# Kernel tuning notes

Hardware: AMD Instinct MI355X
Metric: run time of the kernel (lower is better)

The kernel has to match this reference:

```python
import jax, jax.numpy as jnp
import numpy as np

KS = {0: (6, 18), 1: (4, 12)}


def _build_modal_edges(feat, k_set):
    # feat: [N, C] -> H_modal [N, len(k_set)*N]
    N = feat.shape[0]
    f = feat / jnp.linalg.norm(feat, axis=1, keepdims=True).clip(1e-12)
    sim = f @ f.T  # [N, N] cosine similarity
    H_list = []
    cols_base = jnp.arange(N)
    for k in k_set:
        _, knn = jax.lax.top_k(sim, k + 1)  # [N, k+1]
        rows = knn.reshape(-1)
        cols = jnp.repeat(cols_base, k + 1)
        H = jnp.zeros((N, N), dtype=feat.dtype).at[rows, cols].set(1.0)
        H_list.append(H)
    return jnp.concatenate(H_list, axis=1)


def _build_incidence(feat1, feat2):
    # feat1/feat2: [N, C] (batch-mean features) -> H [2N, 5N]
    N = feat1.shape[0]
    H1 = _build_modal_edges(feat1, KS[0])  # [N, 2N]
    H2 = _build_modal_edges(feat2, KS[1])  # [N, 2N]
    E1, E2 = H1.shape[1], H2.shape[1]
    blk = jnp.concatenate([
        jnp.concatenate([H1, jnp.zeros((N, E2), H1.dtype)], axis=1),
        jnp.concatenate([jnp.zeros((N, E1), H2.dtype), H2], axis=1),
    ], axis=0)  # block_diag -> [2N, 4N]
    eye = jnp.eye(N, dtype=H1.dtype)
    H_inter = jnp.concatenate([eye, eye], axis=0)  # [2N, N]
    return jnp.concatenate([blk, H_inter], axis=1)  # [2N, 5N]


def _hgconv(x, H, W):
    # x: [B, 2N, Fin], H: [2N, E], W: [Fout, Fin] (torch Linear, no bias)
    x = jnp.einsum('bnf,of->bno', x, W)
    DV = H.sum(axis=1).clip(1.0)  # [2N]
    DE = H.sum(axis=0).clip(1.0)  # [E]
    H_norm = H / jnp.sqrt(DV)[:, None] / DE[None, :]
    A = H_norm @ H_norm.T  # [2N, 2N]
    x = jnp.einsum('nm,bmo->bno', A, x)
    return jax.nn.relu(x)


def setup_inputs() -> dict:
    key = jax.random.key(0)
    k1, k2, k3, k4 = jax.random.split(key, 4)
    B, N, C, Hd = 4, 2048, 64, 128
    feat_mod1 = jax.random.normal(k1, (B, N, C), dtype=jnp.float32)
    feat_mod2 = jax.random.normal(k2, (B, N, C), dtype=jnp.float32)
    # xavier_uniform bounds for [out, in]
    b1 = float(np.sqrt(6.0 / (Hd + C)))
    b2 = float(np.sqrt(6.0 / (Hd + Hd)))
    W1 = jax.random.uniform(k3, (Hd, C), minval=-b1, maxval=b1, dtype=jnp.float32)
    W2 = jax.random.uniform(k4, (Hd, Hd), minval=-b2, maxval=b2, dtype=jnp.float32)
    return {"feat_mod1": feat_mod1, "feat_mod2": feat_mod2, "W1": W1, "W2": W2}


def reference(feat_mod1, feat_mod2, W1, W2):
    B, N, _ = feat_mod1.shape
    H = jax.lax.stop_gradient(
        _build_incidence(feat_mod1.mean(axis=0), feat_mod2.mean(axis=0)))
    x = jnp.concatenate([feat_mod1, feat_mod2], axis=1)  # [B, 2N, C]
    x = _hgconv(x, H, W1)
    x = _hgconv(x, H, W2)
    return x[:, :N, :], x[:, N:, :]
```

## Files before the change

kernel.cpp:

```cpp
#include <hip/hip_runtime.h>
#include <math.h>

#define NN 2048
#define TWO_N 4096
#define BB 4
#define CC 64
#define HD 128
#define CANDCAP 32

typedef unsigned short u16;
typedef _Float16 h16;
union H4 { ushort4 u; h16 h[4]; };

__device__ __forceinline__ u16 f2bf(float x) {
    unsigned u = __float_as_uint(x);
    u += 0x7FFFu + ((u >> 16) & 1u);
    return (u16)(u >> 16);
}

__global__ void k_mean_norm(const float* __restrict__ f1, const float* __restrict__ f2,
                            const float* __restrict__ W1, const float* __restrict__ W2,
                            float* __restrict__ g32T, double* __restrict__ gR64,
                            u16* __restrict__ xh,
                            float* __restrict__ W1T, float* __restrict__ W2T,
                            int* __restrict__ DV) {
    int n = blockIdx.x;
    int m = blockIdx.y;
    int c = threadIdx.x;
    if (m == 0 && n < 64) DV[n * 64 + c] = 0;
    if (m == 1) {
        if (n < 128) {
            int idx = n * 64 + c;
            W1T[(size_t)(idx & 63) * HD + (idx >> 6)] = W1[idx];
        } else if (n < 384) {
            int idx = (n - 128) * 64 + c;
            W2T[(size_t)(idx & 127) * HD + (idx >> 7)] = W2[idx];
        }
    }
    const float* f = m ? f2 : f1;
    float xv[BB];
    double s = 0.0;
    for (int b = 0; b < BB; ++b) {
        float v = f[((size_t)(b * NN) + n) * CC + c];
        xv[b] = v; s += (double)v;
    }
    h16* xrow = (h16*)(xh + ((size_t)(m * NN + n)) * (BB * CC));
    for (int b = 0; b < BB; ++b) xrow[b * CC + c] = (h16)xv[b];
    double mean = s * 0.25;
    double sq = mean * mean;
    for (int d = 32; d >= 1; d >>= 1) sq += __shfl_xor(sq, d);
    double norm = sqrt(sq);
    if (norm < 1e-12) norm = 1e-12;
    double g = mean / norm;
    g32T[((size_t)m * CC + c) * NN + n] = (float)g;
    gR64[((size_t)m * NN + n) * CC + c] = g;
}

__global__ void __launch_bounds__(256)
k_sims(const float* __restrict__ g32T, u16* __restrict__ simsbf) {
    __shared__ float As[64 * 64];
    __shared__ float Bs[64 * 64];
    int m  = blockIdx.y;
    int bi = blockIdx.x >> 5, bj = blockIdx.x & 31;
    if (bi > bj) return;
    int i0 = bi * 64, j0 = bj * 64;
    const float* g = g32T + (size_t)m * CC * NN;
    int tid = threadIdx.x;
    #pragma unroll
    for (int q = 0; q < 16; ++q) {
        int idx = q * 256 + tid;
        int k = idx >> 6, r = idx & 63;
        As[k * 64 + r] = g[(size_t)k * NN + i0 + r];
        Bs[k * 64 + r] = g[(size_t)k * NN + j0 + r];
    }
    __syncthreads();
    int tr = tid >> 4, tc = tid & 15;
    float acc[4][4] = {{0.f}};
    #pragma unroll
    for (int k = 0; k < CC; ++k) {
        float4 a = *((const float4*)&As[k * 64 + (tr << 2)]);
        float4 b = *((const float4*)&Bs[k * 64 + (tc << 2)]);
        acc[0][0] += a.x * b.x; acc[0][1] += a.x * b.y; acc[0][2] += a.x * b.z; acc[0][3] += a.x * b.w;
        acc[1][0] += a.y * b.x; acc[1][1] += a.y * b.y; acc[1][2] += a.y * b.z; acc[1][3] += a.y * b.w;
        acc[2][0] += a.z * b.x; acc[2][1] += a.z * b.y; acc[2][2] += a.z * b.z; acc[2][3] += a.z * b.w;
        acc[3][0] += a.w * b.x; acc[3][1] += a.w * b.y; acc[3][2] += a.w * b.z; acc[3][3] += a.w * b.w;
    }
    __syncthreads();
    u16* Cs = (u16*)As;
    u16* srow = simsbf + (size_t)m * NN * NN;
    #pragma unroll
    for (int x = 0; x < 4; ++x) {
        ushort4 vd;
        vd.x = f2bf(acc[x][0]); vd.y = f2bf(acc[x][1]);
        vd.z = f2bf(acc[x][2]); vd.w = f2bf(acc[x][3]);
        *((ushort4*)&srow[(size_t)(i0 + (tr << 2) + x) * NN + j0 + (tc << 2)]) = vd;
        int cr = ((tr << 2) + x) * 66 + (tc << 2);
        Cs[cr + 0] = vd.x; Cs[cr + 1] = vd.y; Cs[cr + 2] = vd.z; Cs[cr + 3] = vd.w;
    }
    __syncthreads();
    #pragma unroll
    for (int q = 0; q < 4; ++q) {
        int idx = q * 256 + tid;
        int cc = idx >> 4, rr4 = (idx & 15) << 2;
        ushort4 vd;
        vd.x = Cs[(rr4 + 0) * 66 + cc];
        vd.y = Cs[(rr4 + 1) * 66 + cc];
        vd.z = Cs[(rr4 + 2) * 66 + cc];
        vd.w = Cs[(rr4 + 3) * 66 + cc];
        *((ushort4*)&srow[(size_t)(j0 + cc) * NN + i0 + rr4]) = vd;
    }
}

__global__ void __launch_bounds__(512)
k_selref(const u16* __restrict__ simsbf, const double* __restrict__ gR64,
         int* __restrict__ knn1, int* __restrict__ knn2, int* __restrict__ DV) {
    __shared__ int    candL[8][CANDCAP];
    __shared__ double dotsL[8][CANDCAP];
    int wave = threadIdx.x >> 6, lane = threadIdx.x & 63;
    int row = blockIdx.x * 8 + wave;
    int m = row >> 11, i = row & 2047;
    int K = m ? 13 : 19;
    const u16* s = simsbf + (size_t)m * NN * NN + (size_t)i * NN;
    float sv[32];
    #pragma unroll
    for (int q = 0; q < 4; ++q) {
        uint4 w = *((const uint4*)(s + q * 512 + (lane << 3)));
        sv[q*8+0] = __uint_as_float(w.x << 16);
        sv[q*8+1] = __uint_as_float(w.x & 0xFFFF0000u);
        sv[q*8+2] = __uint_as_float(w.y << 16);
        sv[q*8+3] = __uint_as_float(w.y & 0xFFFF0000u);
        sv[q*8+4] = __uint_as_float(w.z << 16);
        sv[q*8+5] = __uint_as_float(w.z & 0xFFFF0000u);
        sv[q*8+6] = __uint_as_float(w.w << 16);
        sv[q*8+7] = __uint_as_float(w.w & 0xFFFF0000u);
    }
    float lo = -1.01f, hi = 1.01f;
    for (int it = 0; it < 12; ++it) {
        float t = 0.5f * (lo + hi);
        int c = 0;
        #pragma unroll
        for (int r = 0; r < 32; ++r)
            c += __popcll(__ballot(sv[r] >= t));
        if (c >= K) lo = t; else hi = t;
    }
    float thr = lo - 6e-3f;
    unsigned long long ltmask = (lane == 0) ? 0ull : ((~0ull) >> (64 - lane));
    int base = 0;
    #pragma unroll
    for (int r = 0; r < 32; ++r) {
        int j = ((r >> 3) << 9) + (lane << 3) + (r & 7);
        bool p = sv[r] >= thr;
        unsigned long long mk = __ballot(p);
        int ofs = base + __popcll(mk & ltmask);
        if (p && ofs < CANDCAP) candL[wave][ofs] = j;
        base += __popcll(mk);
    }
    int cnt = (base < CANDCAP) ? base : CANDCAP;
    __syncthreads();
    const double* gm = gR64 + (size_t)m * NN * CC;
    double qc = gm[(size_t)i * CC + lane];
    int t4 = 0;
    for (; t4 + 3 < cnt; t4 += 4) {
        int j0c = candL[wave][t4 + 0], j1c = candL[wave][t4 + 1];
        int j2c = candL[wave][t4 + 2], j3c = candL[wave][t4 + 3];
        double p0 = qc * gm[(size_t)j0c * CC + lane];
        double p1 = qc * gm[(size_t)j1c * CC + lane];
        double p2 = qc * gm[(size_t)j2c * CC + lane];
        double p3 = qc * gm[(size_t)j3c * CC + lane];
        #pragma unroll
        for (int d = 32; d >= 1; d >>= 1) {
            p0 += __shfl_xor(p0, d); p1 += __shfl_xor(p1, d);
            p2 += __shfl_xor(p2, d); p3 += __shfl_xor(p3, d);
        }
        if (lane == 0) {
            dotsL[wave][t4 + 0] = p0; dotsL[wave][t4 + 1] = p1;
            dotsL[wave][t4 + 2] = p2; dotsL[wave][t4 + 3] = p3;
        }
    }
    for (; t4 < cnt; ++t4) {
        int j = candL[wave][t4];
        double p = qc * gm[(size_t)j * CC + lane];
        #pragma unroll
        for (int d = 32; d >= 1; d >>= 1) p += __shfl_xor(p, d);
        if (lane == 0) dotsL[wave][t4] = p;
    }
    __syncthreads();
    int* knn = m ? knn2 : knn1;
    if (lane < cnt) {
        double vt = dotsL[wave][lane]; int jt = candL[wave][lane];
        int rank = 0;
        for (int s2 = 0; s2 < cnt; ++s2) {
            double vs = dotsL[wave][s2]; int js = candL[wave][s2];
            if (vs > vt || (vs == vt && js < jt)) ++rank;
        }
        if (rank < K) {
            knn[(size_t)i * K + rank] = jt;
            int w = (rank < (m ? 5 : 7)) ? 2 : 1;
            atomicAdd(&DV[m ? NN + jt : jt], w);
        }
    }
}

__global__ void k_scan(const int* __restrict__ DV, int* __restrict__ offs,
                       int* __restrict__ cursor, float* __restrict__ dvisf) {
    int lane = threadIdx.x;
    int base = lane * 64;
    int s = 0;
    for (int q = 0; q < 64; ++q) s += DV[base + q];
    int x = s;
    for (int d = 1; d < 64; d <<= 1) {
        int y = __shfl_up(x, d);
        if (lane >= d) x += y;
    }
    int run = x - s;
    for (int q = 0; q < 64; ++q) {
        int v = base + q;
        offs[v] = run; cursor[v] = run;
        dvisf[v] = (float)(1.0 / sqrt((double)(DV[v] + 1)));
        run += DV[v];
    }
    if (lane == 63) offs[TWO_N] = run;
}

__global__ void k_fill(const int* __restrict__ knn1, const int* __restrict__ knn2,
                       int* __restrict__ cursor, int* __restrict__ entries) {
    int id = blockIdx.x * blockDim.x + threadIdx.x;
    const int M1 = NN * 19, M2 = NN * 13;
    if (id < M1) {
        int i = id / 19, t = id % 19;
        int v = knn1[id];
        int p = atomicAdd(&cursor[v], 1); entries[p] = NN + i;
        if (t < 7) { int p2 = atomicAdd(&cursor[v], 1); entries[p2] = i; }
    } else if (id < M1 + M2) {
        int id2 = id - M1;
        int i = id2 / 13, t = id2 % 13;
        int v = NN + knn2[id2];
        int p = atomicAdd(&cursor[v], 1); entries[p] = 3 * NN + i;
        if (t < 5) { int p2 = atomicAdd(&cursor[v], 1); entries[p2] = 2 * NN + i; }
    }
}

__global__ void k_edgeX(const u16* __restrict__ xh, const float* __restrict__ dvisf,
                        const int* __restrict__ knn1, const int* __restrict__ knn2,
                        u16* __restrict__ uh1) {
    int blk = blockIdx.x;
    int t = threadIdx.x;
    int off = t * 4;
    if (blk < NN) {
        int mv = 0; float wv = 0.f;
        if (t < 19) { mv = knn1[(size_t)blk * 19 + t]; wv = dvisf[mv]; }
        float a0=0,a1=0,a2=0,a3=0;
        #pragma unroll
        for (int q = 0; q < 7; ++q) {
            int mq = __shfl(mv, q); float wq = __shfl(wv, q);
            H4 hv; hv.u = *((const ushort4*)(xh + (size_t)mq * 256 + off));
            a0 += (float)hv.h[0]*wq; a1 += (float)hv.h[1]*wq;
            a2 += (float)hv.h[2]*wq; a3 += (float)hv.h[3]*wq;
        }
        { H4 ho; ho.h[0]=(h16)(a0*(1.f/49.f)); ho.h[1]=(h16)(a1*(1.f/49.f));
          ho.h[2]=(h16)(a2*(1.f/49.f)); ho.h[3]=(h16)(a3*(1.f/49.f));
          *((ushort4*)(uh1 + (size_t)blk * 256 + off)) = ho.u; }
        #pragma unroll
        for (int q = 7; q < 19; ++q) {
            int mq = __shfl(mv, q); float wq = __shfl(wv, q);
            H4 hv; hv.u = *((const ushort4*)(xh + (size_t)mq * 256 + off));
            a0 += (float)hv.h[0]*wq; a1 += (float)hv.h[1]*wq;
            a2 += (float)hv.h[2]*wq; a3 += (float)hv.h[3]*wq;
        }
        { H4 ho; ho.h[0]=(h16)(a0*(1.f/361.f)); ho.h[1]=(h16)(a1*(1.f/361.f));
          ho.h[2]=(h16)(a2*(1.f/361.f)); ho.h[3]=(h16)(a3*(1.f/361.f));
          *((ushort4*)(uh1 + (size_t)(NN + blk) * 256 + off)) = ho.u; }
    } else {
        int i = blk - NN;
        int mv = 0; float wv = 0.f;
        if (t < 13) { mv = knn2[(size_t)i * 13 + t]; wv = dvisf[NN + mv]; }
        float a0=0,a1=0,a2=0,a3=0;
        #pragma unroll
        for (int q = 0; q < 5; ++q) {
            int mq = __shfl(mv, q); float wq = __shfl(wv, q);
            H4 hv; hv.u = *((const ushort4*)(xh + (size_t)(NN + mq) * 256 + off));
            a0 += (float)hv.h[0]*wq; a1 += (float)hv.h[1]*wq;
            a2 += (float)hv.h[2]*wq; a3 += (float)hv.h[3]*wq;
        }
        { H4 ho; ho.h[0]=(h16)(a0*(1.f/25.f)); ho.h[1]=(h16)(a1*(1.f/25.f));
          ho.h[2]=(h16)(a2*(1.f/25.f)); ho.h[3]=(h16)(a3*(1.f/25.f));
          *((ushort4*)(uh1 + (size_t)(2 * NN + i) * 256 + off)) = ho.u; }
        #pragma unroll
        for (int q = 5; q < 13; ++q) {
            int mq = __shfl(mv, q); float wq = __shfl(wv, q);
            H4 hv; hv.u = *((const ushort4*)(xh + (size_t)(NN + mq) * 256 + off));
            a0 += (float)hv.h[0]*wq; a1 += (float)hv.h[1]*wq;
            a2 += (float)hv.h[2]*wq; a3 += (float)hv.h[3]*wq;
        }
        { H4 ho; ho.h[0]=(h16)(a0*(1.f/169.f)); ho.h[1]=(h16)(a1*(1.f/169.f));
          ho.h[2]=(h16)(a2*(1.f/169.f)); ho.h[3]=(h16)(a3*(1.f/169.f));
          *((ushort4*)(uh1 + (size_t)(3 * NN + i) * 256 + off)) = ho.u; }
    }
}

__global__ void k_node1(const u16* __restrict__ uh1,
                        const float* __restrict__ f1, const float* __restrict__ f2,
                        const float* __restrict__ dvisf,
                        const int* __restrict__ offs, const int* __restrict__ entries,
                        u16* __restrict__ aggxh) {
    int v = blockIdx.x;
    int l6 = threadIdx.x;
    int b = l6 >> 4, f4i = l6 & 15;
    int s = offs[v], e_end = offs[v + 1];
    float A0[4] = {0,0,0,0}, A1[4] = {0,0,0,0};
    float A2[4] = {0,0,0,0}, A3[4] = {0,0,0,0};
    int p = s;
    for (; p + 3 < e_end; p += 4) {
        H4 h0, h1, h2, h3;
        h0.u = *((const ushort4*)(uh1 + (size_t)entries[p+0] * 256 + l6 * 4));
        h1.u = *((const ushort4*)(uh1 + (size_t)entries[p+1] * 256 + l6 * 4));
        h2.u = *((const ushort4*)(uh1 + (size_t)entries[p+2] * 256 + l6 * 4));
        h3.u = *((const ushort4*)(uh1 + (size_t)entries[p+3] * 256 + l6 * 4));
        #pragma unroll
        for (int j = 0; j < 4; ++j) {
            A0[j] += (float)h0.h[j]; A1[j] += (float)h1.h[j];
            A2[j] += (float)h2.h[j]; A3[j] += (float)h3.h[j];
        }
    }
    for (; p < e_end; ++p) {
        H4 h0; h0.u = *((const ushort4*)(uh1 + (size_t)entries[p] * 256 + l6 * 4));
        #pragma unroll
        for (int j = 0; j < 4; ++j) A0[j] += (float)h0.h[j];
    }
    float r[4];
    #pragma unroll
    for (int j = 0; j < 4; ++j) r[j] = (A0[j] + A1[j]) + (A2[j] + A3[j]);
    int partner = (v < NN) ? v + NN : v - NN;
    float w0 = dvisf[v], w1 = dvisf[partner];
    const float4* x1 = (const float4*)f1;
    const float4* x2 = (const float4*)f2;
    float4 xv = (v < NN) ? x1[((size_t)(b * NN) + v) * 16 + f4i]
                         : x2[((size_t)(b * NN) + (v - NN)) * 16 + f4i];
    float4 xp = (partner < NN) ? x1[((size_t)(b * NN) + partner) * 16 + f4i]
                               : x2[((size_t)(b * NN) + (partner - NN)) * 16 + f4i];
    r[0] += 0.25f * (xv.x * w0 + xp.x * w1);
    r[1] += 0.25f * (xv.y * w0 + xp.y * w1);
    r[2] += 0.25f * (xv.z * w0 + xp.z * w1);
    r[3] += 0.25f * (xv.w * w0 + xp.w * w1);
    H4 ho;
    #pragma unroll
    for (int j = 0; j < 4; ++j) ho.h[j] = (h16)(r[j] * w0);
    *((ushort4*)(aggxh + (size_t)v * 256 + l6 * 4)) = ho.u;
}

__global__ void __launch_bounds__(256)
k_gemm12(const u16* __restrict__ aggxh,
         const float* __restrict__ W1T, const float* __restrict__ W2T,
         u16* __restrict__ yh) {
    __shared__ float wT[64 * 132];
    __shared__ float xT[64 * 33];
    __shared__ float zT[128 * 33];
    int tid = threadIdx.x;
    int bid = blockIdx.x;
    int v0 = bid * 8, g0 = bid * 32;
    #pragma unroll
    for (int p = 0; p < 32; ++p) {
        int idx = p * 256 + tid;
        wT[(idx >> 7) * 132 + (idx & 127)] = W1T[idx];
    }
    #pragma unroll
    for (int it = 0; it < 2; ++it) {
        int item = it * 256 + tid;
        int vl = item >> 6, l6 = item & 63;
        int b = l6 >> 4, c4 = (l6 & 15) << 2;
        H4 hv; hv.u = *((const ushort4*)(aggxh + (size_t)(v0 + vl) * 256 + l6 * 4));
        int rloc = vl * 4 + b;
        #pragma unroll
        for (int j = 0; j < 4; ++j) xT[(c4 + j) * 33 + rloc] = (float)hv.h[j];
    }
    __syncthreads();
    int tr = tid >> 5, tc = tid & 31;
    int r0 = tr * 4, c0 = tc * 4;
    {
        float acc[4][4] = {{0.f}};
        #pragma unroll
        for (int k = 0; k < CC; ++k) {
            float xr0 = xT[k*33 + r0+0], xr1 = xT[k*33 + r0+1];
            float xr2 = xT[k*33 + r0+2], xr3 = xT[k*33 + r0+3];
            float4 w = *((const float4*)&wT[k * 132 + c0]);
            acc[0][0]+=xr0*w.x; acc[0][1]+=xr0*w.y; acc[0][2]+=xr0*w.z; acc[0][3]+=xr0*w.w;
            acc[1][0]+=xr1*w.x; acc[1][1]+=xr1*w.y; acc[1][2]+=xr1*w.z; acc[1][3]+=xr1*w.w;
            acc[2][0]+=xr2*w.x; acc[2][1]+=xr2*w.y; acc[2][2]+=xr2*w.z; acc[2][3]+=xr2*w.w;
            acc[3][0]+=xr3*w.x; acc[3][1]+=xr3*w.y; acc[3][2]+=xr3*w.z; acc[3][3]+=xr3*w.w;
        }
        #pragma unroll
        for (int i = 0; i < 4; ++i)
            #pragma unroll
            for (int j = 0; j < 4; ++j)
                zT[(c0 + j) * 33 + r0 + i] = fmaxf(acc[i][j], 0.f);
    }
    float acc2[4][4] = {{0.f}};
    for (int kc = 0; kc < 2; ++kc) {
        __syncthreads();
        #pragma unroll
        for (int p = 0; p < 32; ++p) {
            int idx = p * 256 + tid;
            int k = idx >> 7, c = idx & 127;
            wT[k * 132 + c] = W2T[(size_t)(kc * 64 + k) * HD + c];
        }
        __syncthreads();
        #pragma unroll
        for (int k = 0; k < 64; ++k) {
            int kk = kc * 64 + k;
            float zr0 = zT[kk*33 + r0+0], zr1 = zT[kk*33 + r0+1];
            float zr2 = zT[kk*33 + r0+2], zr3 = zT[kk*33 + r0+3];
            float4 w = *((const float4*)&wT[k * 132 + c0]);
            acc2[0][0]+=zr0*w.x; acc2[0][1]+=zr0*w.y; acc2[0][2]+=zr0*w.z; acc2[0][3]+=zr0*w.w;
            acc2[1][0]+=zr1*w.x; acc2[1][1]+=zr1*w.y; acc2[1][2]+=zr1*w.z; acc2[1][3]+=zr1*w.w;
            acc2[2][0]+=zr2*w.x; acc2[2][1]+=zr2*w.y; acc2[2][2]+=zr2*w.z; acc2[2][3]+=zr2*w.w;
            acc2[3][0]+=zr3*w.x; acc2[3][1]+=zr3*w.y; acc2[3][2]+=zr3*w.z; acc2[3][3]+=zr3*w.w;
        }
    }
    #pragma unroll
    for (int i = 0; i < 4; ++i) {
        H4 ho;
        ho.h[0] = (h16)acc2[i][0]; ho.h[1] = (h16)acc2[i][1];
        ho.h[2] = (h16)acc2[i][2]; ho.h[3] = (h16)acc2[i][3];
        *((ushort4*)(yh + (size_t)(g0 + r0 + i) * HD + c0)) = ho.u;
    }
}

__global__ void k_edge2(const u16* __restrict__ yh, const float* __restrict__ dvisf,
                        const int* __restrict__ knn1, const int* __restrict__ knn2,
                        u16* __restrict__ uh2) {
    __shared__ int mem[19];
    __shared__ float wv[19];
    int blk = blockIdx.x;
    int t = threadIdx.x;
    int off = t * 4;
    if (blk < NN) {
        if (t < 19) { int v = knn1[(size_t)blk * 19 + t]; mem[t] = v; wv[t] = dvisf[v]; }
        __syncthreads();
        float a0=0,a1=0,a2=0,a3=0;
        #pragma unroll
        for (int q = 0; q < 7; ++q) {
            float w = wv[q];
            H4 hv; hv.u = *((const ushort4*)(yh + (size_t)mem[q] * 512 + off));
            a0 += (float)hv.h[0]*w; a1 += (float)hv.h[1]*w;
            a2 += (float)hv.h[2]*w; a3 += (float)hv.h[3]*w;
        }
        { H4 ho; ho.h[0]=(h16)(a0*(1.f/49.f)); ho.h[1]=(h16)(a1*(1.f/49.f));
          ho.h[2]=(h16)(a2*(1.f/49.f)); ho.h[3]=(h16)(a3*(1.f/49.f));
          *((ushort4*)(uh2 + (size_t)blk * 512 + off)) = ho.u; }
        #pragma unroll
        for (int q = 7; q < 19; ++q) {
            float w = wv[q];
            H4 hv; hv.u = *((const ushort4*)(yh + (size_t)mem[q] * 512 + off));
            a0 += (float)hv.h[0]*w; a1 += (float)hv.h[1]*w;
            a2 += (float)hv.h[2]*w; a3 += (float)hv.h[3]*w;
        }
        { H4 ho; ho.h[0]=(h16)(a0*(1.f/361.f)); ho.h[1]=(h16)(a1*(1.f/361.f));
          ho.h[2]=(h16)(a2*(1.f/361.f)); ho.h[3]=(h16)(a3*(1.f/361.f));
          *((ushort4*)(uh2 + (size_t)(NN + blk) * 512 + off)) = ho.u; }
    } else {
        int i = blk - NN;
        if (t < 13) { int v = NN + knn2[(size_t)i * 13 + t]; mem[t] = v; wv[t] = dvisf[v]; }
        __syncthreads();
        float a0=0,a1=0,a2=0,a3=0;
        #pragma unroll
        for (int q = 0; q < 5; ++q) {
            float w = wv[q];
            H4 hv; hv.u = *((const ushort4*)(yh + (size_t)mem[q] * 512 + off));
            a0 += (float)hv.h[0]*w; a1 += (float)hv.h[1]*w;
            a2 += (float)hv.h[2]*w; a3 += (float)hv.h[3]*w;
        }
        { H4 ho; ho.h[0]=(h16)(a0*(1.f/25.f)); ho.h[1]=(h16)(a1*(1.f/25.f));
          ho.h[2]=(h16)(a2*(1.f/25.f)); ho.h[3]=(h16)(a3*(1.f/25.f));
          *((ushort4*)(uh2 + (size_t)(2 * NN + i) * 512 + off)) = ho.u; }
        #pragma unroll
        for (int q = 5; q < 13; ++q) {
            float w = wv[q];
            H4 hv; hv.u = *((const ushort4*)(yh + (size_t)mem[q] * 512 + off));
            a0 += (float)hv.h[0]*w; a1 += (float)hv.h[1]*w;
            a2 += (float)hv.h[2]*w; a3 += (float)hv.h[3]*w;
        }
        { H4 ho; ho.h[0]=(h16)(a0*(1.f/169.f)); ho.h[1]=(h16)(a1*(1.f/169.f));
          ho.h[2]=(h16)(a2*(1.f/169.f)); ho.h[3]=(h16)(a3*(1.f/169.f));
          *((ushort4*)(uh2 + (size_t)(3 * NN + i) * 512 + off)) = ho.u; }
    }
}

__global__ void k_node2(const u16* __restrict__ uh2, const u16* __restrict__ yh,
                        const float* __restrict__ dvisf,
                        const int* __restrict__ offs, const int* __restrict__ entries,
                        float* __restrict__ out) {
    int v = blockIdx.x;
    int t = threadIdx.x;
    int off = t * 4;
    int s = offs[v], e_end = offs[v + 1];
    float A0[4] = {0,0,0,0}, A1[4] = {0,0,0,0};
    float A2[4] = {0,0,0,0}, A3[4] = {0,0,0,0};
    int p = s;
    for (; p + 3 < e_end; p += 4) {
        H4 h0, h1, h2, h3;
        h0.u = *((const ushort4*)(uh2 + (size_t)entries[p+0] * 512 + off));
        h1.u = *((const ushort4*)(uh2 + (size_t)entries[p+1] * 512 + off));
        h2.u = *((const ushort4*)(uh2 + (size_t)entries[p+2] * 512 + off));
        h3.u = *((const ushort4*)(uh2 + (size_t)entries[p+3] * 512 + off));
        #pragma unroll
        for (int j = 0; j < 4; ++j) {
            A0[j] += (float)h0.h[j]; A1[j] += (float)h1.h[j];
            A2[j] += (float)h2.h[j]; A3[j] += (float)h3.h[j];
        }
    }
    for (; p < e_end; ++p) {
        H4 h0; h0.u = *((const ushort4*)(uh2 + (size_t)entries[p] * 512 + off));
        #pragma unroll
        for (int j = 0; j < 4; ++j) A0[j] += (float)h0.h[j];
    }
    float r[4];
    #pragma unroll
    for (int j = 0; j < 4; ++j) r[j] = (A0[j] + A1[j]) + (A2[j] + A3[j]);
    int partner = (v < NN) ? v + NN : v - NN;
    float w0 = dvisf[v], w1 = dvisf[partner];
    H4 yv, yp;
    yv.u = *((const ushort4*)(yh + (size_t)v * 512 + off));
    yp.u = *((const ushort4*)(yh + (size_t)partner * 512 + off));
    #pragma unroll
    for (int j = 0; j < 4; ++j) {
        r[j] += 0.25f * ((float)yv.h[j] * w0 + (float)yp.h[j] * w1);
        r[j] = fmaxf(r[j] * w0, 0.f);
    }
    int b = t >> 5, f4i = t & 31;
    size_t o4;
    if (v < NN) o4 = ((size_t)(b * NN + v)) * 32 + f4i;
    else        o4 = (size_t)BB * NN * 32 + ((size_t)(b * NN + (v - NN))) * 32 + f4i;
    ((float4*)out)[o4] = make_float4(r[0], r[1], r[2], r[3]);
}

extern "C" void kernel_launch(void* const* d_in, const int* in_sizes, int n_in,
                              void* d_out, int out_size, void* d_ws, size_t ws_size,
                              hipStream_t stream) {
    const float* f1 = (const float*)d_in[0];
    const float* f2 = (const float*)d_in[1];
    const float* W1 = (const float*)d_in[2];
    const float* W2 = (const float*)d_in[3];
    float* out = (float*)d_out;

    char* ws = (char*)d_ws;
    size_t off = 0;
    auto alloc = [&](size_t bytes) -> void* {
        void* p = ws + off;
        off = (off + bytes + 255) & ~(size_t)255;
        return p;
    };
    float*  g32T   = (float*)alloc((size_t)2 * CC * NN * 4);
    double* gR64   = (double*)alloc((size_t)2 * NN * CC * 8);
    u16*    simsbf = (u16*)alloc((size_t)2 * NN * NN * 2);
    u16*    xh     = (u16*)alloc((size_t)TWO_N * BB * CC * 2);
    u16*    uh1    = (u16*)alloc((size_t)4 * NN * BB * CC * 2);
    u16*    aggxh  = (u16*)alloc((size_t)TWO_N * BB * CC * 2);
    u16*    yh     = (u16*)alloc((size_t)TWO_N * BB * HD * 2);
    u16*    uh2    = (u16*)alloc((size_t)4 * NN * BB * HD * 2);
    float*  W1T    = (float*)alloc((size_t)CC * HD * 4);
    float*  W2T    = (float*)alloc((size_t)HD * HD * 4);
    float*  dvisf  = (float*)alloc((size_t)TWO_N * 4);
    int*    knn1   = (int*)alloc((size_t)NN * 19 * 4);
    int*    knn2   = (int*)alloc((size_t)NN * 13 * 4);
    int*    DV     = (int*)alloc((size_t)TWO_N * 4);
    int*    offs   = (int*)alloc((size_t)(TWO_N + 1) * 4);
    int*    cursor = (int*)alloc((size_t)TWO_N * 4);
    int*    entries= (int*)alloc((size_t)(NN * 26 + NN * 18) * 4);

    k_mean_norm<<<dim3(NN, 2), 64, 0, stream>>>(f1, f2, W1, W2, g32T, gR64,
                                                xh, W1T, W2T, DV);
    k_sims<<<dim3(32 * 32, 2), 256, 0, stream>>>(g32T, simsbf);
    k_selref<<<TWO_N / 8, 512, 0, stream>>>(simsbf, gR64, knn1, knn2, DV);
    k_scan<<<1, 64, 0, stream>>>(DV, offs, cursor, dvisf);
    k_fill<<<(NN * 19 + NN * 13 + 255) / 256, 256, 0, stream>>>(knn1, knn2, cursor, entries);

    k_edgeX<<<2 * NN, 64, 0, stream>>>(xh, dvisf, knn1, knn2, uh1);
    k_node1<<<TWO_N, 64, 0, stream>>>(uh1, f1, f2, dvisf, offs, entries, aggxh);
    k_gemm12<<<(BB * TWO_N) / 32, 256, 0, stream>>>(aggxh, W1T, W2T, yh);

    k_edge2<<<2 * NN, 128, 0, stream>>>(yh, dvisf, knn1, knn2, uh2);
    k_node2<<<TWO_N, 128, 0, stream>>>(uh2, yh, dvisf, offs, entries, out);
}
```

Baseline: 188.8 us.

## Use MFMA f16 for the weight GEMMs and fuse scan/fill into neighbouring kernels

The two chained weight GEMMs are rewritten to use the 16x16x32 f16 MFMA instruction, with the weights stored as f16 in their original [out,in] layout instead of transposed f32 tiles in shared memory. The degree scan moves into the last-finishing block of the top-k selection kernel through an atomic done counter. The CSR fill runs as extra blocks of the edge-aggregation kernel. Together these remove two kernel launches and the scalar FMA GEMM loops, at the cost of f16 weight precision. The fused fill runs concurrently with blocks that read knn, which is safe because that kernel never reads entries.

```diff
diff --git a/kernel.cpp b/kernel.cpp
--- a/kernel.cpp
+++ b/kernel.cpp
@@ -11,6 +11,8 @@
 typedef unsigned short u16;
 typedef _Float16 h16;
 union H4 { ushort4 u; h16 h[4]; };
+typedef _Float16 h16v8 __attribute__((ext_vector_type(8)));
+typedef float f32v4 __attribute__((ext_vector_type(4)));
 
 __device__ __forceinline__ u16 f2bf(float x) {
     unsigned u = __float_as_uint(x);
@@ -22,19 +24,20 @@
                             const float* __restrict__ W1, const float* __restrict__ W2,
                             float* __restrict__ g32T, double* __restrict__ gR64,
                             u16* __restrict__ xh,
-                            float* __restrict__ W1T, float* __restrict__ W2T,
-                            int* __restrict__ DV) {
+                            u16* __restrict__ W1h, u16* __restrict__ W2h,
+                            int* __restrict__ DV, int* __restrict__ done) {
     int n = blockIdx.x;
     int m = blockIdx.y;
     int c = threadIdx.x;
     if (m == 0 && n < 64) DV[n * 64 + c] = 0;
+    if (m == 0 && n == 64 && c == 0) *done = 0;
     if (m == 1) {
         if (n < 128) {
             int idx = n * 64 + c;
-            W1T[(size_t)(idx & 63) * HD + (idx >> 6)] = W1[idx];
+            ((h16*)W1h)[idx] = (h16)W1[idx];
         } else if (n < 384) {
             int idx = (n - 128) * 64 + c;
-            W2T[(size_t)(idx & 127) * HD + (idx >> 7)] = W2[idx];
+            ((h16*)W2h)[idx] = (h16)W2[idx];
         }
     }
     const float* f = m ? f2 : f1;
@@ -113,9 +116,14 @@
 
 __global__ void __launch_bounds__(512)
 k_selref(const u16* __restrict__ simsbf, const double* __restrict__ gR64,
-         int* __restrict__ knn1, int* __restrict__ knn2, int* __restrict__ DV) {
+         int* __restrict__ knn1, int* __restrict__ knn2, int* __restrict__ DV,
+         int* __restrict__ done, int* __restrict__ offs,
+         int* __restrict__ cursor, float* __restrict__ dvisf) {
     __shared__ int    candL[8][CANDCAP];
     __shared__ double dotsL[8][CANDCAP];
+    __shared__ int    scanbuf[TWO_N];
+    __shared__ int    wsum[8];
+    __shared__ int    lastFlag;
     int wave = threadIdx.x >> 6, lane = threadIdx.x & 63;
     int row = blockIdx.x * 8 + wave;
     int m = row >> 11, i = row & 2047;
@@ -199,52 +207,66 @@
             atomicAdd(&DV[m ? NN + jt : jt], w);
         }
     }
-}
-
-__global__ void k_scan(const int* __restrict__ DV, int* __restrict__ offs,
-                       int* __restrict__ cursor, float* __restrict__ dvisf) {
-    int lane = threadIdx.x;
-    int base = lane * 64;
-    int s = 0;
-    for (int q = 0; q < 64; ++q) s += DV[base + q];
-    int x = s;
-    for (int d = 1; d < 64; d <<= 1) {
-        int y = __shfl_up(x, d);
-        if (lane >= d) x += y;
-    }
-    int run = x - s;
-    for (int q = 0; q < 64; ++q) {
-        int v = base + q;
-        offs[v] = run; cursor[v] = run;
-        dvisf[v] = (float)(1.0 / sqrt((double)(DV[v] + 1)));
-        run += DV[v];
-    }
-    if (lane == 63) offs[TWO_N] = run;
-}
-
-__global__ void k_fill(const int* __restrict__ knn1, const int* __restrict__ knn2,
-                       int* __restrict__ cursor, int* __restrict__ entries) {
-    int id = blockIdx.x * blockDim.x + threadIdx.x;
-    const int M1 = NN * 19, M2 = NN * 13;
-    if (id < M1) {
-        int i = id / 19, t = id % 19;
-        int v = knn1[id];
-        int p = atomicAdd(&cursor[v], 1); entries[p] = NN + i;
-        if (t < 7) { int p2 = atomicAdd(&cursor[v], 1); entries[p2] = i; }
-    } else if (id < M1 + M2) {
-        int id2 = id - M1;
-        int i = id2 / 13, t = id2 % 13;
-        int v = NN + knn2[id2];
-        int p = atomicAdd(&cursor[v], 1); entries[p] = 3 * NN + i;
-        if (t < 5) { int p2 = atomicAdd(&cursor[v], 1); entries[p2] = 2 * NN + i; }
-    }
-}
-
-__global__ void k_edgeX(const u16* __restrict__ xh, const float* __restrict__ dvisf,
-                        const int* __restrict__ knn1, const int* __restrict__ knn2,
-                        u16* __restrict__ uh1) {
+    __syncthreads();
+    if (threadIdx.x == 0) {
+        int d = __hip_atomic_fetch_add(done, 1, __ATOMIC_ACQ_REL,
+                                       __HIP_MEMORY_SCOPE_AGENT);
+        lastFlag = (d == (int)gridDim.x - 1);
+    }
+    __syncthreads();
+    if (lastFlag) {
+        int t = threadIdx.x;
+        #pragma unroll
+        for (int q = 0; q < 8; ++q) scanbuf[q * 512 + t] = DV[q * 512 + t];
+        __syncthreads();
+        int loc[8]; int sum = 0;
+        #pragma unroll
+        for (int q = 0; q < 8; ++q) { loc[q] = scanbuf[t * 8 + q]; sum += loc[q]; }
+        int x = sum;
+        #pragma unroll
+        for (int d = 1; d < 64; d <<= 1) {
+            int y = __shfl_up(x, d);
+            if (lane >= d) x += y;
+        }
+        if (lane == 63) wsum[t >> 6] = x;
+        __syncthreads();
+        int wp = 0;
+        for (int w = 0; w < (t >> 6); ++w) wp += wsum[w];
+        int run = wp + x - sum;
+        #pragma unroll
+        for (int q = 0; q < 8; ++q) {
+            int v = t * 8 + q;
+            offs[v] = run; cursor[v] = run;
+            dvisf[v] = (float)(1.0 / sqrt((double)(loc[q] + 1)));
+            run += loc[q];
+        }
+        if (t == 511) offs[TWO_N] = run;
+    }
+}
+
+__global__ void k_edgeXfill(const u16* __restrict__ xh, const float* __restrict__ dvisf,
+                            const int* __restrict__ knn1, const int* __restrict__ knn2,
+                            int* __restrict__ cursor, int* __restrict__ entries,
+                            u16* __restrict__ uh1) {
     int blk = blockIdx.x;
     int t = threadIdx.x;
+    if (blk >= TWO_N) {
+        int id = (blk - TWO_N) * 64 + t;
+        const int M1 = NN * 19;
+        if (id < M1) {
+            int i = id / 19, tt = id % 19;
+            int v = knn1[id];
+            int p = atomicAdd(&cursor[v], 1); entries[p] = NN + i;
+            if (tt < 7) { int p2 = atomicAdd(&cursor[v], 1); entries[p2] = i; }
+        } else {
+            int id2 = id - M1;
+            int i = id2 / 13, tt = id2 % 13;
+            int v = NN + knn2[id2];
+            int p = atomicAdd(&cursor[v], 1); entries[p] = 3 * NN + i;
+            if (tt < 5) { int p2 = atomicAdd(&cursor[v], 1); entries[p2] = 2 * NN + i; }
+        }
+        return;
+    }
     int off = t * 4;
     if (blk < NN) {
         int mv = 0; float wv = 0.f;
@@ -350,79 +372,57 @@
 
 __global__ void __launch_bounds__(256)
 k_gemm12(const u16* __restrict__ aggxh,
-         const float* __restrict__ W1T, const float* __restrict__ W2T,
+         const u16* __restrict__ W1h, const u16* __restrict__ W2h,
          u16* __restrict__ yh) {
-    __shared__ float wT[64 * 132];
-    __shared__ float xT[64 * 33];
-    __shared__ float zT[128 * 33];
+    __shared__ h16 zh[32 * 136];
     int tid = threadIdx.x;
     int bid = blockIdx.x;
-    int v0 = bid * 8, g0 = bid * 32;
-    #pragma unroll
-    for (int p = 0; p < 32; ++p) {
-        int idx = p * 256 + tid;
-        wT[(idx >> 7) * 132 + (idx & 127)] = W1T[idx];
-    }
-    #pragma unroll
-    for (int it = 0; it < 2; ++it) {
-        int item = it * 256 + tid;
-        int vl = item >> 6, l6 = item & 63;
-        int b = l6 >> 4, c4 = (l6 & 15) << 2;
-        H4 hv; hv.u = *((const ushort4*)(aggxh + (size_t)(v0 + vl) * 256 + l6 * 4));
-        int rloc = vl * 4 + b;
-        #pragma unroll
-        for (int j = 0; j < 4; ++j) xT[(c4 + j) * 33 + rloc] = (float)hv.h[j];
-    }
-    __syncthreads();
-    int tr = tid >> 5, tc = tid & 31;
-    int r0 = tr * 4, c0 = tc * 4;
-    {
-        float acc[4][4] = {{0.f}};
-        #pragma unroll
-        for (int k = 0; k < CC; ++k) {
-            float xr0 = xT[k*33 + r0+0], xr1 = xT[k*33 + r0+1];
-            float xr2 = xT[k*33 + r0+2], xr3 = xT[k*33 + r0+3];
-            float4 w = *((const float4*)&wT[k * 132 + c0]);
-            acc[0][0]+=xr0*w.x; acc[0][1]+=xr0*w.y; acc[0][2]+=xr0*w.z; acc[0][3]+=xr0*w.w;
-            acc[1][0]+=xr1*w.x; acc[1][1]+=xr1*w.y; acc[1][2]+=xr1*w.z; acc[1][3]+=xr1*w.w;
-            acc[2][0]+=xr2*w.x; acc[2][1]+=xr2*w.y; acc[2][2]+=xr2*w.z; acc[2][3]+=xr2*w.w;
-            acc[3][0]+=xr3*w.x; acc[3][1]+=xr3*w.y; acc[3][2]+=xr3*w.z; acc[3][3]+=xr3*w.w;
-        }
+    int g0 = bid * 32;
+    int wid = tid >> 6, lane = tid & 63;
+    int waveM = wid >> 1, waveN = wid & 1;
+    int r0 = waveM * 16, c0 = waveN * 64;
+    int lrow = lane & 15, lk8 = lane >> 4;
+    const h16* aggp = (const h16*)aggxh;
+    const h16* w1p  = (const h16*)W1h;
+    const h16* w2p  = (const h16*)W2h;
+    f32v4 acc[4] = {{0.f,0.f,0.f,0.f},{0.f,0.f,0.f,0.f},
+                    {0.f,0.f,0.f,0.f},{0.f,0.f,0.f,0.f}};
+    #pragma unroll
+    for (int ks = 0; ks < 2; ++ks) {
+        int kb = ks * 32 + lk8 * 8;
+        h16v8 a = *((const h16v8*)(aggp + (size_t)(g0 + r0 + lrow) * CC + kb));
+        #pragma unroll
+        for (int cb = 0; cb < 4; ++cb) {
+            h16v8 b = *((const h16v8*)(w1p + (size_t)(c0 + cb * 16 + lrow) * CC + kb));
+            acc[cb] = __builtin_amdgcn_mfma_f32_16x16x32_f16(a, b, acc[cb], 0, 0, 0);
+        }
+    }
+    #pragma unroll
+    for (int cb = 0; cb < 4; ++cb)
         #pragma unroll
         for (int i = 0; i < 4; ++i)
-            #pragma unroll
-            for (int j = 0; j < 4; ++j)
-                zT[(c0 + j) * 33 + r0 + i] = fmaxf(acc[i][j], 0.f);
-    }
-    float acc2[4][4] = {{0.f}};
-    for (int kc = 0; kc < 2; ++kc) {
-        __syncthreads();
-        #pragma unroll
-        for (int p = 0; p < 32; ++p) {
-            int idx = p * 256 + tid;
-            int k = idx >> 7, c = idx & 127;
-            wT[k * 132 + c] = W2T[(size_t)(kc * 64 + k) * HD + c];
-        }
-        __syncthreads();
-        #pragma unroll
-        for (int k = 0; k < 64; ++k) {
-            int kk = kc * 64 + k;
-            float zr0 = zT[kk*33 + r0+0], zr1 = zT[kk*33 + r0+1];
-            float zr2 = zT[kk*33 + r0+2], zr3 = zT[kk*33 + r0+3];
-            float4 w = *((const float4*)&wT[k * 132 + c0]);
-            acc2[0][0]+=zr0*w.x; acc2[0][1]+=zr0*w.y; acc2[0][2]+=zr0*w.z; acc2[0][3]+=zr0*w.w;
-            acc2[1][0]+=zr1*w.x; acc2[1][1]+=zr1*w.y; acc2[1][2]+=zr1*w.z; acc2[1][3]+=zr1*w.w;
-            acc2[2][0]+=zr2*w.x; acc2[2][1]+=zr2*w.y; acc2[2][2]+=zr2*w.z; acc2[2][3]+=zr2*w.w;
-            acc2[3][0]+=zr3*w.x; acc2[3][1]+=zr3*w.y; acc2[3][2]+=zr3*w.z; acc2[3][3]+=zr3*w.w;
-        }
-    }
-    #pragma unroll
-    for (int i = 0; i < 4; ++i) {
-        H4 ho;
-        ho.h[0] = (h16)acc2[i][0]; ho.h[1] = (h16)acc2[i][1];
-        ho.h[2] = (h16)acc2[i][2]; ho.h[3] = (h16)acc2[i][3];
-        *((ushort4*)(yh + (size_t)(g0 + r0 + i) * HD + c0)) = ho.u;
-    }
+            zh[(r0 + lk8 * 4 + i) * 136 + c0 + cb * 16 + lrow] =
+                (h16)fmaxf(acc[cb][i], 0.f);
+    __syncthreads();
+    f32v4 acc2[4] = {{0.f,0.f,0.f,0.f},{0.f,0.f,0.f,0.f},
+                     {0.f,0.f,0.f,0.f},{0.f,0.f,0.f,0.f}};
+    #pragma unroll
+    for (int ks = 0; ks < 4; ++ks) {
+        int kb = ks * 32 + lk8 * 8;
+        h16v8 a = *((const h16v8*)(zh + (size_t)(r0 + lrow) * 136 + kb));
+        #pragma unroll
+        for (int cb = 0; cb < 4; ++cb) {
+            h16v8 b = *((const h16v8*)(w2p + (size_t)(c0 + cb * 16 + lrow) * HD + kb));
+            acc2[cb] = __builtin_amdgcn_mfma_f32_16x16x32_f16(a, b, acc2[cb], 0, 0, 0);
+        }
+    }
+    h16* yp = (h16*)yh;
+    #pragma unroll
+    for (int cb = 0; cb < 4; ++cb)
+        #pragma unroll
+        for (int i = 0; i < 4; ++i)
+            yp[(size_t)(g0 + r0 + lk8 * 4 + i) * HD + c0 + cb * 16 + lrow] =
+                (h16)acc2[cb][i];
 }
 
 __global__ void k_edge2(const u16* __restrict__ yh, const float* __restrict__ dvisf,
@@ -557,26 +557,27 @@
     u16*    aggxh  = (u16*)alloc((size_t)TWO_N * BB * CC * 2);
     u16*    yh     = (u16*)alloc((size_t)TWO_N * BB * HD * 2);
     u16*    uh2    = (u16*)alloc((size_t)4 * NN * BB * HD * 2);
-    float*  W1T    = (float*)alloc((size_t)CC * HD * 4);
-    float*  W2T    = (float*)alloc((size_t)HD * HD * 4);
+    u16*    W1h    = (u16*)alloc((size_t)CC * HD * 2);
+    u16*    W2h    = (u16*)alloc((size_t)HD * HD * 2);
     float*  dvisf  = (float*)alloc((size_t)TWO_N * 4);
     int*    knn1   = (int*)alloc((size_t)NN * 19 * 4);
     int*    knn2   = (int*)alloc((size_t)NN * 13 * 4);
     int*    DV     = (int*)alloc((size_t)TWO_N * 4);
+    int*    done   = (int*)alloc(256);
     int*    offs   = (int*)alloc((size_t)(TWO_N + 1) * 4);
     int*    cursor = (int*)alloc((size_t)TWO_N * 4);
     int*    entries= (int*)alloc((size_t)(NN * 26 + NN * 18) * 4);
 
     k_mean_norm<<<dim3(NN, 2), 64, 0, stream>>>(f1, f2, W1, W2, g32T, gR64,
-                                                xh, W1T, W2T, DV);
+                                                xh, W1h, W2h, DV, done);
     k_sims<<<dim3(32 * 32, 2), 256, 0, stream>>>(g32T, simsbf);
-    k_selref<<<TWO_N / 8, 512, 0, stream>>>(simsbf, gR64, knn1, knn2, DV);
-    k_scan<<<1, 64, 0, stream>>>(DV, offs, cursor, dvisf);
-    k_fill<<<(NN * 19 + NN * 13 + 255) / 256, 256, 0, stream>>>(knn1, knn2, cursor, entries);
-
-    k_edgeX<<<2 * NN, 64, 0, stream>>>(xh, dvisf, knn1, knn2, uh1);
+    k_selref<<<TWO_N / 8, 512, 0, stream>>>(simsbf, gR64, knn1, knn2, DV,
+                                            done, offs, cursor, dvisf);
+    k_edgeXfill<<<TWO_N + 1024, 64, 0, stream>>>(xh, dvisf, knn1, knn2,
+                                                 cursor, entries, uh1);
+
     k_node1<<<TWO_N, 64, 0, stream>>>(uh1, f1, f2, dvisf, offs, entries, aggxh);
-    k_gemm12<<<(BB * TWO_N) / 32, 256, 0, stream>>>(aggxh, W1T, W2T, yh);
+    k_gemm12<<<(BB * TWO_N) / 32, 256, 0, stream>>>(aggxh, W1h, W2h, yh);
 
     k_edge2<<<2 * NN, 128, 0, stream>>>(yh, dvisf, knn1, knn2, uh2);
     k_node2<<<TWO_N, 128, 0, stream>>>(uh2, yh, dvisf, offs, entries, out);
```

Result: faster. 171.4 us (-9.2%).
